# Optimization experiments

Measured on AMD Instinct MI355X. Metric: run time of the kernel, lower is better.

## Reference

```python
import jax, jax.numpy as jnp
import numpy as np

SEQ_D = 1024   # sequence_state_dim
PAIR_D = 128   # pairwise_state_dim
H_SEQ = 32     # sequence heads (SEQ_D // 32)
HW = 32        # sequence head width
INNER = PAIR_D // 2  # SequenceToPair inner dim
B, L = 1, 512


def ln(x, g, b):
    m = jnp.mean(x, axis=-1, keepdims=True)
    v = jnp.var(x, axis=-1, keepdims=True)
    return (x - m) * jax.lax.rsqrt(v + 1e-5) * g + b


def setup_inputs() -> dict:
    key = jax.random.key(0)
    ks = jax.random.split(key, 24)
    rn = lambda k, shape, s=0.02: (jax.random.normal(k, shape, jnp.float32) * s)
    inp = {
        "sequence_state": jax.random.normal(ks[0], (B, L, SEQ_D), jnp.float32),
        "pairwise_state": jax.random.normal(ks[1], (B, L, L, PAIR_D), jnp.float32),
        # PairToSequence
        "ln_p2s_g": jnp.ones(PAIR_D), "ln_p2s_b": jnp.zeros(PAIR_D),
        "W_p2s": rn(ks[2], (H_SEQ, PAIR_D)),
        # layernorm_1
        "ln1_g": jnp.ones(SEQ_D), "ln1_b": jnp.zeros(SEQ_D),
        # Attention (gated)
        "Wqkv": rn(ks[3], (3 * SEQ_D, SEQ_D)),
        "Wo": rn(ks[4], (SEQ_D, SEQ_D)), "bo": jnp.zeros(SEQ_D),
        "Wg": rn(ks[5], (SEQ_D, SEQ_D)), "bg": jnp.ones(SEQ_D),
        # mlp_seq
        "ln_s_g": jnp.ones(SEQ_D), "ln_s_b": jnp.zeros(SEQ_D),
        "Wm1": rn(ks[6], (4 * SEQ_D, SEQ_D)), "bm1": jnp.zeros(4 * SEQ_D),
        "Wm2": rn(ks[7], (SEQ_D, 4 * SEQ_D)), "bm2": jnp.zeros(SEQ_D),
        # SequenceToPair
        "ln_sp_g": jnp.ones(SEQ_D), "ln_sp_b": jnp.zeros(SEQ_D),
        "Wsp": rn(ks[8], (2 * INNER, SEQ_D)), "bsp": jnp.zeros(2 * INNER),
        "Wspo": rn(ks[9], (PAIR_D, 2 * INNER)), "bspo": jnp.zeros(PAIR_D),
        # mlp_pair
        "ln_mp_g": jnp.ones(PAIR_D), "ln_mp_b": jnp.zeros(PAIR_D),
        "Wp1": rn(ks[10], (4 * PAIR_D, PAIR_D)), "bp1": jnp.zeros(4 * PAIR_D),
        "Wp2": rn(ks[11], (PAIR_D, 4 * PAIR_D)), "bp2": jnp.zeros(PAIR_D),
        "mask": jnp.ones((B, L), bool),
    }
    return inp


def reference(sequence_state, pairwise_state,
              ln_p2s_g, ln_p2s_b, W_p2s,
              ln1_g, ln1_b, Wqkv, Wo, bo, Wg, bg,
              ln_s_g, ln_s_b, Wm1, bm1, Wm2, bm2,
              ln_sp_g, ln_sp_b, Wsp, bsp, Wspo, bspo,
              ln_mp_g, ln_mp_b, Wp1, bp1, Wp2, bp2,
              mask):
    b, l, _ = sequence_state.shape
    # PairToSequence: pairwise bias  (B, L, L, H)
    bias = ln(pairwise_state, ln_p2s_g, ln_p2s_b) @ W_p2s.T

    # Gated self-attention with pairwise bias
    y = ln(sequence_state, ln1_g, ln1_b)
    t = (y @ Wqkv.T).reshape(b, l, H_SEQ, 3 * HW).transpose(0, 2, 1, 3)  # b h l 3c
    q, k, v = jnp.split(t, 3, axis=-1)
    a = jnp.einsum('bhqc,bhkc->bhqk', q * (HW ** -0.5), k)
    a = a + bias.transpose(0, 3, 1, 2)            # bias: b lq lk h -> b h lq lk
    a = jnp.where(mask[:, None, None, :], a, -jnp.inf)
    a = jax.nn.softmax(a, axis=-1)
    o = jnp.einsum('bhqk,bhkc->bqhc', a, v).reshape(b, l, SEQ_D)
    o = jax.nn.sigmoid(y @ Wg.T + bg) * o         # gate computed from layernormed input
    o = o @ Wo.T + bo
    s = sequence_state + o

    # mlp_seq residual
    s = s + (jax.nn.relu(ln(s, ln_s_g, ln_s_b) @ Wm1.T + bm1) @ Wm2.T + bm2)

    # SequenceToPair: outer-product-style pair update
    sp = ln(s, ln_sp_g, ln_sp_b) @ Wsp.T + bsp    # b l 2*inner
    qh, kh = jnp.split(sp, 2, axis=-1)
    prod = qh[:, None, :, :] * kh[:, :, None, :]  # b l l inner
    diff = qh[:, None, :, :] - kh[:, :, None, :]
    pz = jnp.concatenate([prod, diff], axis=-1) @ Wspo.T + bspo
    p = pairwise_state + pz

    # mlp_pair residual
    p = p + (jax.nn.relu(ln(p, ln_mp_g, ln_mp_b) @ Wp1.T + bp1) @ Wp2.T + bp2)
    return (s, p)
```

## Files before the change

### kernel.cpp

```cpp
#include <hip/hip_runtime.h>
#include <hip/hip_bf16.h>
#include <cstddef>


#define L 512
#define SEQ_D 1024
#define PAIR_D 128
#define NH 32
#define HW 32

typedef short bf16x8 __attribute__((ext_vector_type(8)));
typedef float f32x4 __attribute__((ext_vector_type(4)));
typedef unsigned short ushort_t;

__device__ inline float wred_sum(float v) {
#pragma unroll
  for (int off = 32; off; off >>= 1) v += __shfl_xor(v, off, 64);
  return v;
}
__device__ inline unsigned pk2(float a, float b) {
  unsigned r;
  asm("v_cvt_pk_bf16_f32 %0, %1, %2" : "=v"(r) : "v"(a), "v"(b));
  return r;
}
__device__ inline ushort_t bf1(float a) {
  unsigned r;
  asm("v_cvt_pk_bf16_f32 %0, %1, %2" : "=v"(r) : "v"(a), "v"(0.f));
  return (ushort_t)r;
}
__device__ inline float bfl(unsigned u) { return __uint_as_float(u << 16); }
__device__ inline float bfh(unsigned u) { return __uint_as_float(u & 0xffff0000u); }
__device__ inline float bfu(ushort_t u) { return __uint_as_float((unsigned)u << 16); }

#define SWZ(row, kb) ((((row)) << 8) + ((kb) ^ (((row)&7) << 4)))
#define SWZ64(row, kb) ((((row)) << 7) + ((kb) ^ (((row)&7) << 4)))

__device__ __forceinline__ void stage_w32k(const ushort_t* __restrict__ src,
                                           int row_stride, int col_off,
                                           char* lds, int w, int l) {
#pragma unroll
  for (int i = 0; i < 8; ++i) {
    const int o = w * 8192 + i * 1024 + l * 16;
    const int row = o >> 8;
    const int kb = (o & 255) ^ (((row) & 7) << 4);
    const ushort_t* g = src + (size_t)row * row_stride + col_off + (kb >> 1);
    __builtin_amdgcn_global_load_lds(
        (const __attribute__((address_space(1))) unsigned int*)g,
        (__attribute__((address_space(3))) unsigned int*)(lds + w * 8192 + i * 1024),
        16, 0, 0);
  }
}

__global__ __launch_bounds__(256) void cvt9_kernel(
    const float* __restrict__ s0, ushort_t* __restrict__ d0,
    const float* __restrict__ s1, ushort_t* __restrict__ d1,
    const float* __restrict__ s2, ushort_t* __restrict__ d2,
    const float* __restrict__ s3, ushort_t* __restrict__ d3,
    const float* __restrict__ s4, ushort_t* __restrict__ d4,
    const float* __restrict__ s5, ushort_t* __restrict__ d5,
    const float* __restrict__ s6, ushort_t* __restrict__ d6,
    const float* __restrict__ s7, ushort_t* __restrict__ d7,
    const float* __restrict__ s8, ushort_t* __restrict__ d8,
    const float* __restrict__ bgate, float* __restrict__ bias_cat) {
  const int b = blockIdx.x;
  if (b >= 6792) {
    const int i = (b - 6792) * 256 + threadIdx.x;
    bias_cat[i] = (i < 3072) ? 0.f : bgate[i - 3072];
    return;
  }
  if (b >= 6728) {
    const float* s; ushort_t* d; int base, rowlen;
    if (b < 6760) { s = s7; d = d7; base = b - 6728; rowlen = 128; }
    else          { s = s8; d = d8; base = b - 6760; rowlen = 512; }
    const int i = base * 256 + threadIdx.x;
    float4 a = ((const float4*)s)[2 * i], c = ((const float4*)s)[2 * i + 1];
    const int fe = i * 8;
    const int row = fe / rowlen;
    const int fk = fe % rowlen;
    const int ch = fk >> 7, k0 = fk & 127;
    const int kk = k0 >> 5, r0 = k0 & 31;
    const int hi = (r0 >> 4) & 1, g16a = (r0 >> 2) & 3;
    const int p1 = kk * 32 + g16a * 8 + hi * 4;
    ushort_t* dst = d + (size_t)row * rowlen + ch * 128;
    uint2 w1; w1.x = pk2(a.x, a.y); w1.y = pk2(a.z, a.w);
    uint2 w2; w2.x = pk2(c.x, c.y); w2.y = pk2(c.z, c.w);
    *(uint2*)(dst + p1) = w1;
    *(uint2*)(dst + p1 + 8) = w2;
    return;
  }
  const float* s; ushort_t* d; int base;
  if (b < 1536)      { s = s0; d = d0; base = b; }
  else if (b < 2048) { s = s1; d = d1; base = b - 1536; }
  else if (b < 2560) { s = s2; d = d2; base = b - 2048; }
  else if (b < 4608) { s = s3; d = d3; base = b - 2560; }
  else if (b < 6656) { s = s4; d = d4; base = b - 4608; }
  else if (b < 6720) { s = s5; d = d5; base = b - 6656; }
  else               { s = s6; d = d6; base = b - 6720; }
  const int i = base * 256 + threadIdx.x;
  float4 a = ((const float4*)s)[2 * i], c = ((const float4*)s)[2 * i + 1];
  uint4 w;
  w.x = pk2(a.x, a.y); w.y = pk2(a.z, a.w);
  w.z = pk2(c.x, c.y); w.w = pk2(c.z, c.w);
  ((uint4*)d)[i] = w;
}

__global__ __launch_bounds__(256) void ln1024b_kernel(
    const float* __restrict__ in, const float* __restrict__ g,
    const float* __restrict__ b, ushort_t* __restrict__ out) {
  const int row = blockIdx.x;
  const int tid = threadIdx.x;
  float4 v = ((const float4*)(in + (size_t)row * SEQ_D))[tid];
  float s = v.x + v.y + v.z + v.w;
  float s2 = v.x * v.x + v.y * v.y + v.z * v.z + v.w * v.w;
  __shared__ float red[8];
  const int lane = tid & 63, wid = tid >> 6;
  s = wred_sum(s);
  s2 = wred_sum(s2);
  if (lane == 0) { red[wid] = s; red[4 + wid] = s2; }
  __syncthreads();
  s = red[0] + red[1] + red[2] + red[3];
  s2 = red[4] + red[5] + red[6] + red[7];
  const float mean = s * (1.0f / SEQ_D);
  const float var = s2 * (1.0f / SEQ_D) - mean * mean;
  const float rstd = rsqrtf(var + 1e-5f);
  float4 gv = ((const float4*)g)[tid];
  float4 bv = ((const float4*)b)[tid];
  const float o0 = (v.x - mean) * rstd * gv.x + bv.x;
  const float o1 = (v.y - mean) * rstd * gv.y + bv.y;
  const float o2 = (v.z - mean) * rstd * gv.z + bv.z;
  const float o3 = (v.w - mean) * rstd * gv.w + bv.w;
  uint2 pkd; pkd.x = pk2(o0, o1); pkd.y = pk2(o2, o3);
  ((uint2*)(out + (size_t)row * SEQ_D))[tid] = pkd;
}

template <int BIAS, int RELU, int RES, int OBF16>
__global__ __launch_bounds__(256, 2) void gemm_mfma_kernel(
    const ushort_t* __restrict__ A, const ushort_t* __restrict__ B,
    const float* __restrict__ bias, const float* __restrict__ res,
    float* __restrict__ C, ushort_t* __restrict__ Cb, int M, int N, int K) {
  __shared__ __align__(16) char smem[24576];
  char* Ab = smem;
  char* Bb = smem + 8192;
  const int tid = threadIdx.x;
  const int l = tid & 63, w = tid >> 6;
  const int wr = w >> 1, wc = w & 1;
  const int lane16 = l & 15, g16 = l >> 4;
  const int bm = blockIdx.y * 64, bn = blockIdx.x * 128;
  const f32x4 fz = {0.f, 0.f, 0.f, 0.f};
  f32x4 acc[4][2];
#pragma unroll
  for (int i = 0; i < 4; ++i)
#pragma unroll
    for (int j = 0; j < 2; ++j) acc[i][j] = fz;

  for (int k0 = 0; k0 < K; k0 += 64) {
    __syncthreads();
#pragma unroll
    for (int u = 0; u < 2; ++u) {
      const int slot = u * 256 + tid;
      const int row = slot >> 3, sl = slot & 7;
      bf16x8 v = *(const bf16x8*)(A + (size_t)(bm + row) * K + k0 + sl * 8);
      *(bf16x8*)(Ab + SWZ64(row, sl * 16)) = v;
    }
#pragma unroll
    for (int u = 0; u < 4; ++u) {
      const int slot = u * 256 + tid;
      const int row = slot >> 3, sl = slot & 7;
      bf16x8 v = *(const bf16x8*)(B + (size_t)(bn + row) * K + k0 + sl * 8);
      *(bf16x8*)(Bb + SWZ64(row, sl * 16)) = v;
    }
    __syncthreads();
#pragma unroll
    for (int kk = 0; kk < 2; ++kk) {
      const int kb = kk * 64 + g16 * 16;
      bf16x8 af[2], bf[4];
#pragma unroll
      for (int rb = 0; rb < 2; ++rb) {
        const int row = wr * 32 + rb * 16 + lane16;
        af[rb] = *(const bf16x8*)(Ab + SWZ64(row, kb));
      }
#pragma unroll
      for (int cb = 0; cb < 4; ++cb) {
        const int row = wc * 64 + cb * 16 + lane16;
        bf[cb] = *(const bf16x8*)(Bb + SWZ64(row, kb));
      }
#pragma unroll
      for (int cb = 0; cb < 4; ++cb)
#pragma unroll
        for (int rb = 0; rb < 2; ++rb)
          acc[cb][rb] = __builtin_amdgcn_mfma_f32_16x16x32_bf16(
              bf[cb], af[rb], acc[cb][rb], 0, 0, 0);
    }
  }
#pragma unroll
  for (int cb = 0; cb < 4; ++cb) {
    const int col0 = bn + wc * 64 + cb * 16 + g16 * 4;
    float4 bi = make_float4(0.f, 0.f, 0.f, 0.f);
    if (BIAS) bi = *(const float4*)(bias + col0);
#pragma unroll
    for (int rb = 0; rb < 2; ++rb) {
      const int row = bm + wr * 32 + rb * 16 + lane16;
      f32x4 v = acc[cb][rb];
      v[0] += bi.x; v[1] += bi.y; v[2] += bi.z; v[3] += bi.w;
      if (RELU) {
        v[0] = fmaxf(v[0], 0.f); v[1] = fmaxf(v[1], 0.f);
        v[2] = fmaxf(v[2], 0.f); v[3] = fmaxf(v[3], 0.f);
      }
      if (RES) {
        const float4 r4 = *(const float4*)(res + (size_t)row * N + col0);
        v[0] += r4.x; v[1] += r4.y; v[2] += r4.z; v[3] += r4.w;
      }
      if (OBF16) {
        uint2 pkd; pkd.x = pk2(v[0], v[1]); pkd.y = pk2(v[2], v[3]);
        *(uint2*)(Cb + (size_t)row * N + col0) = pkd;
      } else {
        float4 o4; o4.x = v[0]; o4.y = v[1]; o4.z = v[2]; o4.w = v[3];
        *(float4*)(C + (size_t)row * N + col0) = o4;
      }
    }
  }
}

__global__ __launch_bounds__(256) void p2s_mfma_kernel(
    const float* __restrict__ pair, const float* __restrict__ g,
    const float* __restrict__ b, const float* __restrict__ W,
    ushort_t* __restrict__ biasTb) {
  __shared__ __align__(16) char pnb[32768];
  __shared__ __align__(16) char wls[8192];
  const int tid = threadIdx.x;
  const int l = tid & 63, w = tid >> 6;
  const int lane16 = l & 15, g16 = l >> 4;
  const size_t r0 = (size_t)blockIdx.x * 128;
  const int i_idx = (int)(r0 >> 9), j0 = (int)(r0 & 511);
#pragma unroll
  for (int u = 0; u < 2; ++u) {
    const int slot = u * 256 + tid;
    const int row = slot >> 4, sl = slot & 15;
    const float4 v0 = *(const float4*)(W + (size_t)row * 128 + sl * 8);
    const float4 v1 = *(const float4*)(W + (size_t)row * 128 + sl * 8 + 4);
    uint4 wv; wv.x = pk2(v0.x, v0.y); wv.y = pk2(v0.z, v0.w);
    wv.z = pk2(v1.x, v1.y); wv.w = pk2(v1.z, v1.w);
    *(uint4*)(wls + SWZ(row, sl * 16)) = wv;
  }
  {
    const int l32 = tid & 31, rg = tid >> 5;
    const float4 gv = *(const float4*)(g + l32 * 4);
    const float4 bv = *(const float4*)(b + l32 * 4);
#pragma unroll
    for (int it = 0; it < 16; ++it) {
      const int r = it * 8 + rg;
      const float4 v = *(const float4*)(pair + (r0 + r) * 128 + l32 * 4);
      float s = v.x + v.y + v.z + v.w;
      float s2 = v.x * v.x + v.y * v.y + v.z * v.z + v.w * v.w;
#pragma unroll
      for (int off = 1; off < 32; off <<= 1) {
        s += __shfl_xor(s, off, 64);
        s2 += __shfl_xor(s2, off, 64);
      }
      const float mean = s * (1.0f / 128.0f);
      const float rstd = rsqrtf(s2 * (1.0f / 128.0f) - mean * mean + 1e-5f);
      const float n0 = (v.x - mean) * rstd * gv.x + bv.x;
      const float n1 = (v.y - mean) * rstd * gv.y + bv.y;
      const float n2 = (v.z - mean) * rstd * gv.z + bv.z;
      const float n3 = (v.w - mean) * rstd * gv.w + bv.w;
      uint2 pkd; pkd.x = pk2(n0, n1); pkd.y = pk2(n2, n3);
      *(uint2*)(pnb + SWZ(r, l32 * 8)) = pkd;
    }
  }
  __syncthreads();
  const f32x4 fz = {0.f, 0.f, 0.f, 0.f};
  f32x4 a2[2][2];
#pragma unroll
  for (int i = 0; i < 2; ++i)
#pragma unroll
    for (int j = 0; j < 2; ++j) a2[i][j] = fz;
#pragma unroll
  for (int kk = 0; kk < 4; ++kk) {
    bf16x8 wf[2], pf[2];
#pragma unroll
    for (int hb = 0; hb < 2; ++hb)
      wf[hb] = *(const bf16x8*)(wls + SWZ(hb * 16 + lane16, kk * 64 + g16 * 16));
#pragma unroll
    for (int rb = 0; rb < 2; ++rb)
      pf[rb] = *(const bf16x8*)(pnb + SWZ(w * 32 + rb * 16 + lane16, kk * 64 + g16 * 16));
#pragma unroll
    for (int hb = 0; hb < 2; ++hb)
#pragma unroll
      for (int rb = 0; rb < 2; ++rb)
        a2[hb][rb] = __builtin_amdgcn_mfma_f32_16x16x32_bf16(
            wf[hb], pf[rb], a2[hb][rb], 0, 0, 0);
  }
#pragma unroll
  for (int hb = 0; hb < 2; ++hb)
#pragma unroll
    for (int rb = 0; rb < 2; ++rb) {
      const int j = j0 + w * 32 + rb * 16 + lane16;
#pragma unroll
      for (int qq = 0; qq < 4; ++qq) {
        const int hh = hb * 16 + g16 * 4 + qq;
        biasTb[((size_t)hh * 512 + i_idx) * 512 + j] = bf1(a2[hb][rb][qq]);
      }
    }
}

__global__ __launch_bounds__(256) void attn_kernel(
    const ushort_t* __restrict__ tb, const ushort_t* __restrict__ biasTb,
    ushort_t* __restrict__ ob) {
  __shared__ __align__(16) ushort_t Vt[32][80];
  const int tid = threadIdx.x;
  const int l = tid & 63, wq = tid >> 6;
  const int lane16 = l & 15, g16 = l >> 4;
  const int h = blockIdx.y;
  const int q = blockIdx.x * 64 + wq * 16 + lane16;
  const float scale = 0.17677669529663689f;
  const bf16x8 qf = *(const bf16x8*)(tb + (size_t)q * 4096 + h * 96 + g16 * 8);
  const ushort_t* brow = biasTb + ((size_t)h * 512 + q) * 512;
  float m = -3e38f, lsum = 0.f;
  const f32x4 fz = {0.f, 0.f, 0.f, 0.f};
  f32x4 accp[2] = {fz, fz};
  for (int kt = 0; kt < 512; kt += 64) {
    {
      const int kr = tid >> 2, cc = tid & 3;
      bf16x8 vv = *(const bf16x8*)(tb + (size_t)(kt + kr) * 4096 + h * 96 + 64 + cc * 8);
#pragma unroll
      for (int u = 0; u < 8; ++u) Vt[cc * 8 + u][kr] = (ushort_t)vv[u];
    }
    __syncthreads();
    f32x4 st[4];
#pragma unroll
    for (int kb = 0; kb < 4; ++kb) {
      const bf16x8 kf = *(const bf16x8*)(
          tb + (size_t)(kt + kb * 16 + lane16) * 4096 + h * 96 + 32 + g16 * 8);
      st[kb] = __builtin_amdgcn_mfma_f32_16x16x32_bf16(kf, qf, fz, 0, 0, 0);
      const ushort4 bv = *(const ushort4*)(brow + kt + kb * 16 + g16 * 4);
      st[kb][0] = st[kb][0] * scale + bfu(bv.x);
      st[kb][1] = st[kb][1] * scale + bfu(bv.y);
      st[kb][2] = st[kb][2] * scale + bfu(bv.z);
      st[kb][3] = st[kb][3] * scale + bfu(bv.w);
    }
    float tm = st[0][0];
#pragma unroll
    for (int kb = 0; kb < 4; ++kb)
#pragma unroll
      for (int qq = 0; qq < 4; ++qq) tm = fmaxf(tm, st[kb][qq]);
    tm = fmaxf(tm, __shfl_xor(tm, 16, 64));
    tm = fmaxf(tm, __shfl_xor(tm, 32, 64));
    const float mn = fmaxf(m, tm);
    const float corr = __expf(m - mn);
    m = mn;
    lsum *= corr;
#pragma unroll
    for (int ct = 0; ct < 2; ++ct) {
      accp[ct][0] *= corr; accp[ct][1] *= corr;
      accp[ct][2] *= corr; accp[ct][3] *= corr;
    }
#pragma unroll
    for (int kb = 0; kb < 4; ++kb)
#pragma unroll
      for (int qq = 0; qq < 4; ++qq) {
        const float e = __expf(st[kb][qq] - mn);
        st[kb][qq] = e;
        lsum += e;
      }
    const int src0 = lane16 + ((l & 16) << 1);
    const int src1 = src0 + 16;
    const bool hi = (l & 32) != 0;
#pragma unroll
    for (int kk = 0; kk < 2; ++kk) {
      float lo4[4], hi4[4];
#pragma unroll
      for (int qq = 0; qq < 4; ++qq) {
        const float a0 = __shfl(st[kk * 2][qq], src0, 64);
        const float a1 = __shfl(st[kk * 2][qq], src1, 64);
        const float b0 = __shfl(st[kk * 2 + 1][qq], src0, 64);
        const float b1 = __shfl(st[kk * 2 + 1][qq], src1, 64);
        lo4[qq] = hi ? b0 : a0;
        hi4[qq] = hi ? b1 : a1;
      }
      uint4 pu;
      pu.x = pk2(lo4[0], lo4[1]); pu.y = pk2(lo4[2], lo4[3]);
      pu.z = pk2(hi4[0], hi4[1]); pu.w = pk2(hi4[2], hi4[3]);
      bf16x8 pf;
      __builtin_memcpy(&pf, &pu, 16);
#pragma unroll
      for (int ct = 0; ct < 2; ++ct) {
        const bf16x8 vf = *(const bf16x8*)&Vt[ct * 16 + lane16][kk * 32 + g16 * 8];
        accp[ct] = __builtin_amdgcn_mfma_f32_16x16x32_bf16(vf, pf, accp[ct], 0, 0, 0);
      }
    }
    __syncthreads();
  }
  lsum += __shfl_xor(lsum, 16, 64);
  lsum += __shfl_xor(lsum, 32, 64);
  const float inv = 1.0f / lsum;
#pragma unroll
  for (int ct = 0; ct < 2; ++ct) {
    const int col = h * 32 + ct * 16 + g16 * 4;
    const ushort4 gv = *(const ushort4*)(tb + (size_t)q * 4096 + 3072 + col);
    float4 o4;
    o4.x = accp[ct][0] * inv * (1.0f / (1.0f + __expf(-bfu(gv.x))));
    o4.y = accp[ct][1] * inv * (1.0f / (1.0f + __expf(-bfu(gv.y))));
    o4.z = accp[ct][2] * inv * (1.0f / (1.0f + __expf(-bfu(gv.z))));
    o4.w = accp[ct][3] * inv * (1.0f / (1.0f + __expf(-bfu(gv.w))));
    uint2 pkd; pkd.x = pk2(o4.x, o4.y); pkd.y = pk2(o4.z, o4.w);
    *(uint2*)(ob + (size_t)q * SEQ_D + col) = pkd;
  }
}

__global__ __launch_bounds__(256, 2) void pairfuse64_kernel(
    const float* __restrict__ spb, const ushort_t* __restrict__ Wspob,
    const float* __restrict__ bspo, const float* __restrict__ pairw,
    const float* __restrict__ lng, const float* __restrict__ lnb,
    const ushort_t* __restrict__ Wp1b, const float* __restrict__ bp1,
    const ushort_t* __restrict__ Wp2b, const float* __restrict__ bp2,
    float* __restrict__ pout) {
  __shared__ __align__(16) char Wbuf[65536];
  char* buf0 = Wbuf;
  char* buf1 = Wbuf + 32768;
  const int tid = threadIdx.x;
  const int l = tid & 63, w = tid >> 6;
  const int lane16 = l & 15, g16 = l >> 4;
  const size_t r0 = (size_t)blockIdx.x * 128;
  const int i_idx = (int)(r0 >> 9), j0 = (int)(r0 & 511);
  size_t grow[2];
  grow[0] = r0 + w * 32 + lane16;
  grow[1] = grow[0] + 16;

  stage_w32k(Wspob, 128, 0, buf0, w, l);
  stage_w32k(Wp1b, 128, 0, buf1, w, l);

  bf16x8 xf[2][4];
  {
    const float* krow = spb + (size_t)i_idx * 128 + 64;
#pragma unroll
    for (int rb = 0; rb < 2; ++rb) {
      const float* qrow = spb + (size_t)(j0 + w * 32 + rb * 16 + lane16) * 128;
#pragma unroll
      for (int kk = 0; kk < 4; ++kk) {
        const int c = ((kk & 1) << 5) + g16 * 8;
        const float4 q0 = *(const float4*)(qrow + c);
        const float4 q1 = *(const float4*)(qrow + c + 4);
        const float4 k0 = *(const float4*)(krow + c);
        const float4 k1 = *(const float4*)(krow + c + 4);
        uint4 u;
        if (kk < 2) {
          u.x = pk2(q0.x * k0.x, q0.y * k0.y);
          u.y = pk2(q0.z * k0.z, q0.w * k0.w);
          u.z = pk2(q1.x * k1.x, q1.y * k1.y);
          u.w = pk2(q1.z * k1.z, q1.w * k1.w);
        } else {
          u.x = pk2(q0.x - k0.x, q0.y - k0.y);
          u.y = pk2(q0.z - k0.z, q0.w - k0.w);
          u.z = pk2(q1.x - k1.x, q1.y - k1.y);
          u.w = pk2(q1.z - k1.z, q1.w - k1.w);
        }
        __builtin_memcpy(&xf[rb][kk], &u, 16);
      }
    }
  }
  __syncthreads();

  const f32x4 fz = {0.f, 0.f, 0.f, 0.f};
  f32x4 acc[2][8];
#pragma unroll
  for (int rb = 0; rb < 2; ++rb)
#pragma unroll
    for (int cb = 0; cb < 8; ++cb) acc[rb][cb] = fz;
#pragma unroll
  for (int cb = 0; cb < 8; ++cb) {
#pragma unroll
    for (int kk = 0; kk < 4; ++kk) {
      const bf16x8 wf = *(const bf16x8*)(
          buf0 + SWZ(cb * 16 + lane16, kk * 64 + g16 * 16));
      acc[0][cb] = __builtin_amdgcn_mfma_f32_16x16x32_bf16(wf, xf[0][kk], acc[0][cb], 0, 0, 0);
      acc[1][cb] = __builtin_amdgcn_mfma_f32_16x16x32_bf16(wf, xf[1][kk], acc[1][cb], 0, 0, 0);
    }
  }

  uint2 Ppk[2][8];
  bf16x8 pnf[2][4];
#pragma unroll
  for (int rb = 0; rb < 2; ++rb) {
    float s = 0.f, s2 = 0.f;
#pragma unroll
    for (int cb = 0; cb < 8; ++cb) {
      const int col0 = cb * 16 + g16 * 4;
      const float4 bs = *(const float4*)(bspo + col0);
      const float4 pw = *(const float4*)(pairw + grow[rb] * 128 + col0);
      acc[rb][cb][0] += bs.x + pw.x; acc[rb][cb][1] += bs.y + pw.y;
      acc[rb][cb][2] += bs.z + pw.z; acc[rb][cb][3] += bs.w + pw.w;
      s += acc[rb][cb][0] + acc[rb][cb][1] + acc[rb][cb][2] + acc[rb][cb][3];
      s2 += acc[rb][cb][0] * acc[rb][cb][0] + acc[rb][cb][1] * acc[rb][cb][1] +
            acc[rb][cb][2] * acc[rb][cb][2] + acc[rb][cb][3] * acc[rb][cb][3];
      Ppk[rb][cb].x = pk2(acc[rb][cb][0], acc[rb][cb][1]);
      Ppk[rb][cb].y = pk2(acc[rb][cb][2], acc[rb][cb][3]);
    }
    s += __shfl_xor(s, 16, 64);  s += __shfl_xor(s, 32, 64);
    s2 += __shfl_xor(s2, 16, 64); s2 += __shfl_xor(s2, 32, 64);
    const float mean = s * (1.0f / 128.0f);
    const float rstd = rsqrtf(s2 * (1.0f / 128.0f) - mean * mean + 1e-5f);
    uint2 pnpk[8];
#pragma unroll
    for (int cb = 0; cb < 8; ++cb) {
      const int col0 = cb * 16 + g16 * 4;
      const float4 gv = *(const float4*)(lng + col0);
      const float4 bv = *(const float4*)(lnb + col0);
      const float n0 = (acc[rb][cb][0] - mean) * rstd * gv.x + bv.x;
      const float n1 = (acc[rb][cb][1] - mean) * rstd * gv.y + bv.y;
      const float n2 = (acc[rb][cb][2] - mean) * rstd * gv.z + bv.z;
      const float n3 = (acc[rb][cb][3] - mean) * rstd * gv.w + bv.w;
      pnpk[cb].x = pk2(n0, n1); pnpk[cb].y = pk2(n2, n3);
    }
#pragma unroll
    for (int fk = 0; fk < 4; ++fk) {
      uint4 u;
      u.x = pnpk[2 * fk].x;     u.y = pnpk[2 * fk].y;
      u.z = pnpk[2 * fk + 1].x; u.w = pnpk[2 * fk + 1].y;
      __builtin_memcpy(&pnf[rb][fk], &u, 16);
    }
  }

  f32x4 acc2[2][8];
#pragma unroll
  for (int rb = 0; rb < 2; ++rb)
#pragma unroll
    for (int cb = 0; cb < 8; ++cb) acc2[rb][cb] = fz;

  for (int ch = 0; ch < 4; ++ch) {
    __syncthreads();
    stage_w32k(Wp2b, 512, ch * 128, buf0, w, l);
    bf16x8 hf[2][4];
#pragma unroll
    for (int fk = 0; fk < 4; ++fk) {
      uint2 hpk[2][2];
#pragma unroll
      for (int cbl = 0; cbl < 2; ++cbl) {
        const int cb = fk * 2 + cbl;
        f32x4 hacc[2] = {fz, fz};
#pragma unroll
        for (int kk = 0; kk < 4; ++kk) {
          const bf16x8 w1f = *(const bf16x8*)(
              buf1 + SWZ(cb * 16 + lane16, kk * 64 + g16 * 16));
          hacc[0] = __builtin_amdgcn_mfma_f32_16x16x32_bf16(w1f, pnf[0][kk], hacc[0], 0, 0, 0);
          hacc[1] = __builtin_amdgcn_mfma_f32_16x16x32_bf16(w1f, pnf[1][kk], hacc[1], 0, 0, 0);
        }
        const int hcol = ch * 128 + cb * 16 + g16 * 4;
        const float4 bi = *(const float4*)(bp1 + hcol);
#pragma unroll
        for (int rb = 0; rb < 2; ++rb) {
          const float h0 = fmaxf(hacc[rb][0] + bi.x, 0.f);
          const float h1 = fmaxf(hacc[rb][1] + bi.y, 0.f);
          const float h2 = fmaxf(hacc[rb][2] + bi.z, 0.f);
          const float h3 = fmaxf(hacc[rb][3] + bi.w, 0.f);
          hpk[rb][cbl].x = pk2(h0, h1); hpk[rb][cbl].y = pk2(h2, h3);
        }
      }
#pragma unroll
      for (int rb = 0; rb < 2; ++rb) {
        uint4 u;
        u.x = hpk[rb][0].x; u.y = hpk[rb][0].y;
        u.z = hpk[rb][1].x; u.w = hpk[rb][1].y;
        __builtin_memcpy(&hf[rb][fk], &u, 16);
      }
    }
    __syncthreads();
    if (ch < 3) stage_w32k(Wp1b + (size_t)(ch + 1) * 128 * 128, 128, 0, buf1, w, l);
#pragma unroll
    for (int cb = 0; cb < 8; ++cb) {
#pragma unroll
      for (int kk = 0; kk < 4; ++kk) {
        const bf16x8 w2f = *(const bf16x8*)(
            buf0 + SWZ(cb * 16 + lane16, kk * 64 + g16 * 16));
        acc2[0][cb] = __builtin_amdgcn_mfma_f32_16x16x32_bf16(w2f, hf[0][kk], acc2[0][cb], 0, 0, 0);
        acc2[1][cb] = __builtin_amdgcn_mfma_f32_16x16x32_bf16(w2f, hf[1][kk], acc2[1][cb], 0, 0, 0);
      }
    }
  }

#pragma unroll
  for (int rb = 0; rb < 2; ++rb) {
#pragma unroll
    for (int cb = 0; cb < 8; ++cb) {
      const int col0 = cb * 16 + g16 * 4;
      const float4 b2 = *(const float4*)(bp2 + col0);
      float4 o4;
      o4.x = acc2[rb][cb][0] + b2.x + bfl(Ppk[rb][cb].x);
      o4.y = acc2[rb][cb][1] + b2.y + bfh(Ppk[rb][cb].x);
      o4.z = acc2[rb][cb][2] + b2.z + bfl(Ppk[rb][cb].y);
      o4.w = acc2[rb][cb][3] + b2.w + bfh(Ppk[rb][cb].y);
      *(float4*)(pout + grow[rb] * 128 + col0) = o4;
    }
  }
}

extern "C" void kernel_launch(void* const* d_in, const int* in_sizes, int n_in,
                              void* d_out, int out_size, void* d_ws,
                              size_t ws_size, hipStream_t stream) {
  (void)in_sizes; (void)n_in; (void)out_size; (void)ws_size;
  const float* seq      = (const float*)d_in[0];
  const float* pair     = (const float*)d_in[1];
  const float* ln_p2s_g = (const float*)d_in[2];
  const float* ln_p2s_b = (const float*)d_in[3];
  const float* W_p2s    = (const float*)d_in[4];
  const float* ln1_g    = (const float*)d_in[5];
  const float* ln1_b    = (const float*)d_in[6];
  const float* Wqkv     = (const float*)d_in[7];
  const float* Wo       = (const float*)d_in[8];
  const float* bo       = (const float*)d_in[9];
  const float* Wg       = (const float*)d_in[10];
  const float* bg       = (const float*)d_in[11];
  const float* ln_s_g   = (const float*)d_in[12];
  const float* ln_s_b   = (const float*)d_in[13];
  const float* Wm1      = (const float*)d_in[14];
  const float* bm1      = (const float*)d_in[15];
  const float* Wm2      = (const float*)d_in[16];
  const float* bm2      = (const float*)d_in[17];
  const float* ln_sp_g  = (const float*)d_in[18];
  const float* ln_sp_b  = (const float*)d_in[19];
  const float* Wsp      = (const float*)d_in[20];
  const float* bsp      = (const float*)d_in[21];
  const float* Wspo     = (const float*)d_in[22];
  const float* bspo     = (const float*)d_in[23];
  const float* ln_mp_g  = (const float*)d_in[24];
  const float* ln_mp_b  = (const float*)d_in[25];
  const float* Wp1      = (const float*)d_in[26];
  const float* bp1      = (const float*)d_in[27];
  const float* Wp2      = (const float*)d_in[28];
  const float* bp2      = (const float*)d_in[29];

  float* out_s = (float*)d_out;
  float* out_p = out_s + 512 * 1024;

  float* ws = (float*)d_ws;
  ushort_t* y_b = (ushort_t*)ws;
  ushort_t* t_b = (ushort_t*)(ws + 262144);
  float* s1  = ws + 262144 + 1048576;
  ushort_t* ob  = (ushort_t*)(s1 + 524288);
  ushort_t* h1b = (ushort_t*)(s1 + 524288 + 262144);
  float* spb = s1 + 524288 + 262144 + 1048576;
  ushort_t* wspo_b = (ushort_t*)(spb + 65536);
  ushort_t* wp1_b  = (ushort_t*)(spb + 65536 + 8192);
  ushort_t* wp2_b  = (ushort_t*)(spb + 65536 + 40960);
  float* bias_cat  = spb + 65536 + 73728;

  ushort_t* biasTb = (ushort_t*)out_p;
  ushort_t* wq_b  = (ushort_t*)(out_p + 8388608);
  ushort_t* wg_b  = wq_b + 3145728;
  ushort_t* wo_b  = wg_b + 1048576;
  ushort_t* wm1_b = wo_b + 1048576;
  ushort_t* wm2_b = wm1_b + 4194304;
  ushort_t* wsp_b = wm2_b + 4194304;

  cvt9_kernel<<<6808, 256, 0, stream>>>(Wqkv, wq_b, Wg, wg_b, Wo, wo_b,
                                        Wm1, wm1_b, Wm2, wm2_b, Wsp, wsp_b,
                                        Wspo, wspo_b, Wp1, wp1_b, Wp2, wp2_b,
                                        bg, bias_cat);
  ln1024b_kernel<<<512, 256, 0, stream>>>(seq, ln1_g, ln1_b, y_b);
  gemm_mfma_kernel<1, 0, 0, 1><<<dim3(32, 8), 256, 0, stream>>>(
      y_b, wq_b, bias_cat, nullptr, nullptr, t_b, 512, 4096, 1024);
  p2s_mfma_kernel<<<2048, 256, 0, stream>>>(pair, ln_p2s_g, ln_p2s_b, W_p2s,
                                            biasTb);
  attn_kernel<<<dim3(8, 32), 256, 0, stream>>>(t_b, biasTb, ob);
  gemm_mfma_kernel<1, 0, 1, 0><<<dim3(8, 8), 256, 0, stream>>>(
      ob, wo_b, bo, seq, s1, nullptr, 512, 1024, 1024);
  ln1024b_kernel<<<512, 256, 0, stream>>>(s1, ln_s_g, ln_s_b, y_b);
  gemm_mfma_kernel<1, 1, 0, 1><<<dim3(32, 8), 256, 0, stream>>>(
      y_b, wm1_b, bm1, nullptr, nullptr, h1b, 512, 4096, 1024);
  gemm_mfma_kernel<1, 0, 1, 0><<<dim3(8, 8), 256, 0, stream>>>(
      h1b, wm2_b, bm2, s1, out_s, nullptr, 512, 1024, 4096);
  ln1024b_kernel<<<512, 256, 0, stream>>>(out_s, ln_sp_g, ln_sp_b, y_b);
  gemm_mfma_kernel<1, 0, 0, 0><<<dim3(1, 8), 256, 0, stream>>>(
      y_b, wsp_b, bsp, nullptr, spb, nullptr, 512, 128, 1024);
  pairfuse64_kernel<<<2048, 256, 0, stream>>>(spb, wspo_b, bspo, pair,
                                              ln_mp_g, ln_mp_b, wp1_b, bp1,
                                              wp2_b, bp2, out_p);
}
```

Baseline: 376.4 us.

## Triple-buffer pair MLP weights in 16KB LDS slices to cut LDS and overlap loads

```diff
diff --git a/kernel.cpp b/kernel.cpp
--- a/kernel.cpp
+++ b/kernel.cpp
@@ -35,18 +35,19 @@
 #define SWZ(row, kb) ((((row)) << 8) + ((kb) ^ (((row)&7) << 4)))
 #define SWZ64(row, kb) ((((row)) << 7) + ((kb) ^ (((row)&7) << 4)))
 
-__device__ __forceinline__ void stage_w32k(const ushort_t* __restrict__ src,
+__device__ __forceinline__ void stage_w16k(const ushort_t* __restrict__ src,
                                            int row_stride, int col_off,
-                                           char* lds, int w, int l) {
-#pragma unroll
-  for (int i = 0; i < 8; ++i) {
-    const int o = w * 8192 + i * 1024 + l * 16;
+                                           int row_off, char* lds, int tid) {
+#pragma unroll
+  for (int i = 0; i < 4; ++i) {
+    const int o = i * 4096 + tid * 16;
     const int row = o >> 8;
     const int kb = (o & 255) ^ (((row) & 7) << 4);
-    const ushort_t* g = src + (size_t)row * row_stride + col_off + (kb >> 1);
+    const ushort_t* g =
+        src + (size_t)(row_off + row) * row_stride + col_off + (kb >> 1);
     __builtin_amdgcn_global_load_lds(
         (const __attribute__((address_space(1))) unsigned int*)g,
-        (__attribute__((address_space(3))) unsigned int*)(lds + w * 8192 + i * 1024),
+        (__attribute__((address_space(3))) unsigned int*)(lds + o),
         16, 0, 0);
   }
 }
@@ -407,6 +408,66 @@
   }
 }
 
+#define G0H(BUF, HH)                                                         \
+  _Pragma("unroll") for (int cb4 = 0; cb4 < 4; ++cb4) {                      \
+    _Pragma("unroll") for (int kk = 0; kk < 4; ++kk) {                       \
+      const bf16x8 wf = *(const bf16x8*)((BUF) +                             \
+          SWZ(cb4 * 16 + lane16, kk * 64 + g16 * 16));                       \
+      acc[0][(HH)*4 + cb4] = __builtin_amdgcn_mfma_f32_16x16x32_bf16(        \
+          wf, xf[0][kk], acc[0][(HH)*4 + cb4], 0, 0, 0);                     \
+      acc[1][(HH)*4 + cb4] = __builtin_amdgcn_mfma_f32_16x16x32_bf16(        \
+          wf, xf[1][kk], acc[1][(HH)*4 + cb4], 0, 0, 0);                     \
+    }                                                                        \
+  }
+
+#define G1H(BUF, CH, HH)                                                     \
+  _Pragma("unroll") for (int fkl = 0; fkl < 2; ++fkl) {                      \
+    uint2 hpk[2][2];                                                         \
+    _Pragma("unroll") for (int cbl = 0; cbl < 2; ++cbl) {                    \
+      const int cb4 = fkl * 2 + cbl;                                         \
+      f32x4 hacc0 = fz, hacc1 = fz;                                          \
+      _Pragma("unroll") for (int kk = 0; kk < 4; ++kk) {                     \
+        const bf16x8 w1f = *(const bf16x8*)((BUF) +                          \
+            SWZ(cb4 * 16 + lane16, kk * 64 + g16 * 16));                     \
+        hacc0 = __builtin_amdgcn_mfma_f32_16x16x32_bf16(w1f, pnf[0][kk],     \
+                                                        hacc0, 0, 0, 0);     \
+        hacc1 = __builtin_amdgcn_mfma_f32_16x16x32_bf16(w1f, pnf[1][kk],     \
+                                                        hacc1, 0, 0, 0);     \
+      }                                                                      \
+      const int hcol = (CH) * 128 + ((HH)*4 + cb4) * 16 + g16 * 4;           \
+      const float4 bi = *(const float4*)(bp1 + hcol);                        \
+      hpk[0][cbl].x = pk2(fmaxf(hacc0[0] + bi.x, 0.f),                       \
+                          fmaxf(hacc0[1] + bi.y, 0.f));                      \
+      hpk[0][cbl].y = pk2(fmaxf(hacc0[2] + bi.z, 0.f),                       \
+                          fmaxf(hacc0[3] + bi.w, 0.f));                      \
+      hpk[1][cbl].x = pk2(fmaxf(hacc1[0] + bi.x, 0.f),                       \
+                          fmaxf(hacc1[1] + bi.y, 0.f));                      \
+      hpk[1][cbl].y = pk2(fmaxf(hacc1[2] + bi.z, 0.f),                       \
+                          fmaxf(hacc1[3] + bi.w, 0.f));                      \
+    }                                                                        \
+    {                                                                        \
+      uint4 u0, u1;                                                          \
+      u0.x = hpk[0][0].x; u0.y = hpk[0][0].y;                                \
+      u0.z = hpk[0][1].x; u0.w = hpk[0][1].y;                                \
+      u1.x = hpk[1][0].x; u1.y = hpk[1][0].y;                                \
+      u1.z = hpk[1][1].x; u1.w = hpk[1][1].y;                                \
+      __builtin_memcpy(&hf[0][(HH)*2 + fkl], &u0, 16);                       \
+      __builtin_memcpy(&hf[1][(HH)*2 + fkl], &u1, 16);                       \
+    }                                                                        \
+  }
+
+#define G2H(BUF, HH)                                                         \
+  _Pragma("unroll") for (int cb4 = 0; cb4 < 4; ++cb4) {                      \
+    _Pragma("unroll") for (int kk = 0; kk < 4; ++kk) {                       \
+      const bf16x8 w2f = *(const bf16x8*)((BUF) +                            \
+          SWZ(cb4 * 16 + lane16, kk * 64 + g16 * 16));                       \
+      acc2[0][(HH)*4 + cb4] = __builtin_amdgcn_mfma_f32_16x16x32_bf16(       \
+          w2f, hf[0][kk], acc2[0][(HH)*4 + cb4], 0, 0, 0);                   \
+      acc2[1][(HH)*4 + cb4] = __builtin_amdgcn_mfma_f32_16x16x32_bf16(       \
+          w2f, hf[1][kk], acc2[1][(HH)*4 + cb4], 0, 0, 0);                   \
+    }                                                                        \
+  }
+
 __global__ __launch_bounds__(256, 2) void pairfuse64_kernel(
     const float* __restrict__ spb, const ushort_t* __restrict__ Wspob,
     const float* __restrict__ bspo, const float* __restrict__ pairw,
@@ -414,9 +475,10 @@
     const ushort_t* __restrict__ Wp1b, const float* __restrict__ bp1,
     const ushort_t* __restrict__ Wp2b, const float* __restrict__ bp2,
     float* __restrict__ pout) {
-  __shared__ __align__(16) char Wbuf[65536];
-  char* buf0 = Wbuf;
-  char* buf1 = Wbuf + 32768;
+  __shared__ __align__(16) char Wbuf[49152];
+  char* b0 = Wbuf;
+  char* b1 = Wbuf + 16384;
+  char* b2 = Wbuf + 32768;
   const int tid = threadIdx.x;
   const int l = tid & 63, w = tid >> 6;
   const int lane16 = l & 15, g16 = l >> 4;
@@ -426,8 +488,9 @@
   grow[0] = r0 + w * 32 + lane16;
   grow[1] = grow[0] + 16;
 
-  stage_w32k(Wspob, 128, 0, buf0, w, l);
-  stage_w32k(Wp1b, 128, 0, buf1, w, l);
+  stage_w16k(Wspob, 128, 0, 0, b0, tid);
+  stage_w16k(Wspob, 128, 0, 64, b1, tid);
+  stage_w16k(Wp1b, 128, 0, 0, b2, tid);
 
   bf16x8 xf[2][4];
   {
@@ -466,19 +529,22 @@
   for (int rb = 0; rb < 2; ++rb)
 #pragma unroll
     for (int cb = 0; cb < 8; ++cb) acc[rb][cb] = fz;
-#pragma unroll
-  for (int cb = 0; cb < 8; ++cb) {
-#pragma unroll
-    for (int kk = 0; kk < 4; ++kk) {
-      const bf16x8 wf = *(const bf16x8*)(
-          buf0 + SWZ(cb * 16 + lane16, kk * 64 + g16 * 16));
-      acc[0][cb] = __builtin_amdgcn_mfma_f32_16x16x32_bf16(wf, xf[0][kk], acc[0][cb], 0, 0, 0);
-      acc[1][cb] = __builtin_amdgcn_mfma_f32_16x16x32_bf16(wf, xf[1][kk], acc[1][cb], 0, 0, 0);
-    }
-  }
-
+  bf16x8 pnf[2][4];
+  bf16x8 hf[2][4];
   uint2 Ppk[2][8];
-  bf16x8 pnf[2][4];
+  f32x4 acc2[2][8];
+#pragma unroll
+  for (int rb = 0; rb < 2; ++rb)
+#pragma unroll
+    for (int cb = 0; cb < 8; ++cb) acc2[rb][cb] = fz;
+
+  G0H(b0, 0);
+  __syncthreads();
+  stage_w16k(Wp1b, 128, 0, 64, b0, tid);
+  G0H(b1, 1);
+  __syncthreads();
+  stage_w16k(Wp2b, 512, 0, 0, b1, tid);
+
 #pragma unroll
   for (int rb = 0; rb < 2; ++rb) {
     float s = 0.f, s2 = 0.f;
@@ -520,74 +586,34 @@
     }
   }
 
-  f32x4 acc2[2][8];
-#pragma unroll
-  for (int rb = 0; rb < 2; ++rb)
-#pragma unroll
-    for (int cb = 0; cb < 8; ++cb) acc2[rb][cb] = fz;
-
-  for (int ch = 0; ch < 4; ++ch) {
-    __syncthreads();
-    stage_w32k(Wp2b, 512, ch * 128, buf0, w, l);
-    bf16x8 hf[2][4];
-#pragma unroll
-    for (int fk = 0; fk < 4; ++fk) {
-      uint2 hpk[2][2];
-#pragma unroll
-      for (int cbl = 0; cbl < 2; ++cbl) {
-        const int cb = fk * 2 + cbl;
-        f32x4 hacc[2] = {fz, fz};
-#pragma unroll
-        for (int kk = 0; kk < 4; ++kk) {
-          const bf16x8 w1f = *(const bf16x8*)(
-              buf1 + SWZ(cb * 16 + lane16, kk * 64 + g16 * 16));
-          hacc[0] = __builtin_amdgcn_mfma_f32_16x16x32_bf16(w1f, pnf[0][kk], hacc[0], 0, 0, 0);
-          hacc[1] = __builtin_amdgcn_mfma_f32_16x16x32_bf16(w1f, pnf[1][kk], hacc[1], 0, 0, 0);
-        }
-        const int hcol = ch * 128 + cb * 16 + g16 * 4;
-        const float4 bi = *(const float4*)(bp1 + hcol);
-#pragma unroll
-        for (int rb = 0; rb < 2; ++rb) {
-          const float h0 = fmaxf(hacc[rb][0] + bi.x, 0.f);
-          const float h1 = fmaxf(hacc[rb][1] + bi.y, 0.f);
-          const float h2 = fmaxf(hacc[rb][2] + bi.z, 0.f);
-          const float h3 = fmaxf(hacc[rb][3] + bi.w, 0.f);
-          hpk[rb][cbl].x = pk2(h0, h1); hpk[rb][cbl].y = pk2(h2, h3);
-        }
-      }
-#pragma unroll
-      for (int rb = 0; rb < 2; ++rb) {
-        uint4 u;
-        u.x = hpk[rb][0].x; u.y = hpk[rb][0].y;
-        u.z = hpk[rb][1].x; u.w = hpk[rb][1].y;
-        __builtin_memcpy(&hf[rb][fk], &u, 16);
-      }
-    }
-    __syncthreads();
-    if (ch < 3) stage_w32k(Wp1b + (size_t)(ch + 1) * 128 * 128, 128, 0, buf1, w, l);
-#pragma unroll
-    for (int cb = 0; cb < 8; ++cb) {
-#pragma unroll
-      for (int kk = 0; kk < 4; ++kk) {
-        const bf16x8 w2f = *(const bf16x8*)(
-            buf0 + SWZ(cb * 16 + lane16, kk * 64 + g16 * 16));
-        acc2[0][cb] = __builtin_amdgcn_mfma_f32_16x16x32_bf16(w2f, hf[0][kk], acc2[0][cb], 0, 0, 0);
-        acc2[1][cb] = __builtin_amdgcn_mfma_f32_16x16x32_bf16(w2f, hf[1][kk], acc2[1][cb], 0, 0, 0);
-      }
-    }
-  }
+  G1H(b2, 0, 0); __syncthreads(); stage_w16k(Wp2b, 512, 0, 64, b2, tid);
+  G1H(b0, 0, 1); __syncthreads(); stage_w16k(Wp1b, 128, 0, 128, b0, tid);
+  G2H(b1, 0);    __syncthreads(); stage_w16k(Wp1b, 128, 0, 192, b1, tid);
+  G2H(b2, 1);    __syncthreads(); stage_w16k(Wp2b, 512, 128, 0, b2, tid);
+  G1H(b0, 1, 0); __syncthreads(); stage_w16k(Wp2b, 512, 128, 64, b0, tid);
+  G1H(b1, 1, 1); __syncthreads(); stage_w16k(Wp1b, 128, 0, 256, b1, tid);
+  G2H(b2, 0);    __syncthreads(); stage_w16k(Wp1b, 128, 0, 320, b2, tid);
+  G2H(b0, 1);    __syncthreads(); stage_w16k(Wp2b, 512, 256, 0, b0, tid);
+  G1H(b1, 2, 0); __syncthreads(); stage_w16k(Wp2b, 512, 256, 64, b1, tid);
+  G1H(b2, 2, 1); __syncthreads(); stage_w16k(Wp1b, 128, 0, 384, b2, tid);
+  G2H(b0, 0);    __syncthreads(); stage_w16k(Wp1b, 128, 0, 448, b0, tid);
+  G2H(b1, 1);    __syncthreads(); stage_w16k(Wp2b, 512, 384, 0, b1, tid);
+  G1H(b2, 3, 0); __syncthreads(); stage_w16k(Wp2b, 512, 384, 64, b2, tid);
+  G1H(b0, 3, 1); __syncthreads();
+  G2H(b1, 0);    __syncthreads();
+  G2H(b2, 1);
 
 #pragma unroll
   for (int rb = 0; rb < 2; ++rb) {
 #pragma unroll
     for (int cb = 0; cb < 8; ++cb) {
       const int col0 = cb * 16 + g16 * 4;
-      const float4 b2 = *(const float4*)(bp2 + col0);
+      const float4 b2v = *(const float4*)(bp2 + col0);
       float4 o4;
-      o4.x = acc2[rb][cb][0] + b2.x + bfl(Ppk[rb][cb].x);
-      o4.y = acc2[rb][cb][1] + b2.y + bfh(Ppk[rb][cb].x);
-      o4.z = acc2[rb][cb][2] + b2.z + bfl(Ppk[rb][cb].y);
-      o4.w = acc2[rb][cb][3] + b2.w + bfh(Ppk[rb][cb].y);
+      o4.x = acc2[rb][cb][0] + b2v.x + bfl(Ppk[rb][cb].x);
+      o4.y = acc2[rb][cb][1] + b2v.y + bfh(Ppk[rb][cb].x);
+      o4.z = acc2[rb][cb][2] + b2v.z + bfl(Ppk[rb][cb].y);
+      o4.w = acc2[rb][cb][3] + b2v.w + bfh(Ppk[rb][cb].y);
       *(float4*)(pout + grow[rb] * 128 + col0) = o4;
     }
   }
```

Measured after the change: 387.7 us. +3.0%, slower.
